# Kernel optimization log

Hardware: AMD Instinct MI355X
Metric: run time of the kernel (lower is better)

Reference implementation:

```python
import jax, jax.numpy as jnp
import numpy as np
import math

D_MODEL = 512
EXPAND = 2
D_INNER = EXPAND * D_MODEL          # 1024
HEADDIM = 8
NHEADS = D_INNER // HEADDIM         # 128
NGROUPS = 2
D_STATE = 16
CONV_DIM = D_INNER + 2 * NGROUPS * D_STATE   # 1088
D_IN_PROJ = 2 * D_INNER + 2 * NGROUPS * D_STATE + NHEADS  # 2240
P13 = [(0, 0), (1, 1)]
P31 = [(1, 1), (0, 0)]
P33 = [(1, 1), (1, 1)]


def silu(x):
    return x * jax.nn.sigmoid(x)


def dwconv(x, w, pad):
    # depthwise 2D conv; x: (B,C,H,W), w: (C,1,kh,kw)
    return jax.lax.conv_general_dilated(
        x, w, (1, 1), pad,
        dimension_numbers=('NCHW', 'OIHW', 'NCHW'),
        feature_group_count=x.shape[1])


def interleave_ch(a, b):
    # channel-interleave: out[:, ::2] = a, out[:, 1::2] = b
    Bn, C, Hh, Ww = a.shape
    return jnp.stack([a, b], axis=2).reshape(Bn, 2 * C, Hh, Ww)


def linear_attn(x, dt, A, Bm, Cm, Dp):
    # non-causal linear-attention duality of Mamba2 (grouped heads)
    # x: (B,L,h,p), dt: (B,L,h), A: (h,) negative, Bm/Cm: (B,L,g*ds), Dp: (h,)
    b, L, h, p = x.shape
    g, ds = NGROUPS, D_STATE
    dA = -(dt * A[None, None, :])          # ssd_positive_dA -> positive
    Vs = x * dA[..., None]
    K = Bm.reshape(b, L, g, ds)
    Q = Cm.reshape(b, L, g, ds)
    Vg = Vs.reshape(b, L, h // g, g, p)
    KV = jnp.einsum('blgs,blmgp->bmgsp', K, Vg)       # (b, h/g, g, ds, p)
    y = jnp.einsum('blgs,bmgsp->blmgp', Q, KV)        # (b, L, h/g, g, p)
    y = y + (x * Dp[None, None, :, None]).reshape(b, L, h // g, g, p)
    return y.reshape(b, L, h, p)


def setup_inputs() -> dict:
    key = jax.random.key(0)
    ks = jax.random.split(key, 20)
    Bn, Hh, Ww = 8, 64, 64
    L = Hh * Ww
    u = jax.random.normal(ks[0], (Bn, L, D_MODEL), jnp.float32)
    W_in = jax.random.normal(ks[1], (D_IN_PROJ, D_MODEL), jnp.float32) / math.sqrt(D_MODEL)
    dt = jnp.exp(jax.random.uniform(ks[2], (NHEADS,)) * (math.log(0.1) - math.log(0.001)) + math.log(0.001))
    dt = jnp.clip(dt, 1e-4, None)
    dt_bias = dt + jnp.log(-jnp.expm1(-dt))
    A_log = jnp.log(jax.random.uniform(ks[3], (NHEADS,), minval=1.0, maxval=16.0))
    Dp = jnp.ones((NHEADS,), jnp.float32)

    def cw(k, c, kh, kw):
        return jax.random.normal(k, (c, 1, kh, kw), jnp.float32) / math.sqrt(kh * kw)

    bcC = 2 * NGROUPS * D_STATE // 4  # 16
    w_conv2d = cw(ks[4], CONV_DIM // 2, 3, 3)
    w13x1 = cw(ks[5], D_INNER // 4, 1, 3)
    w31x1 = cw(ks[6], D_INNER // 4, 3, 1)
    w13x2 = cw(ks[7], D_INNER // 4, 1, 3)
    w31x2 = cw(ks[8], D_INNER // 4, 3, 1)
    w13bc1 = cw(ks[9], bcC, 1, 3)
    w31bc1 = cw(ks[10], bcC, 3, 1)
    w13bc2 = cw(ks[11], bcC, 1, 3)
    w31bc2 = cw(ks[12], bcC, 3, 1)
    w_conv2d_z = cw(ks[13], D_INNER, 3, 3)
    ln_g = jnp.ones((D_INNER,), jnp.float32)
    ln_b = jnp.zeros((D_INNER,), jnp.float32)
    scale = jnp.float32(1.0)
    shift = jnp.float32(0.0)
    alpha1 = jnp.float32(1.0)
    alpha2 = jnp.float32(1.0)
    W_out = jax.random.normal(ks[14], (D_MODEL, 2 * D_INNER), jnp.float32) / math.sqrt(2 * D_INNER)
    return dict(u=u, H=Hh, W=Ww, W_in=W_in, dt_bias=dt_bias, A_log=A_log, Dp=Dp,
                w_conv2d=w_conv2d, w13x1=w13x1, w31x1=w31x1, w13x2=w13x2, w31x2=w31x2,
                w13bc1=w13bc1, w31bc1=w31bc1, w13bc2=w13bc2, w31bc2=w31bc2,
                w_conv2d_z=w_conv2d_z, ln_g=ln_g, ln_b=ln_b, scale=scale, shift=shift,
                alpha1=alpha1, alpha2=alpha2, W_out=W_out)


def reference(u, H, W, W_in, dt_bias, A_log, Dp, w_conv2d, w13x1, w31x1, w13x2, w31x2,
              w13bc1, w31bc1, w13bc2, w31bc2, w_conv2d_z, ln_g, ln_b, scale, shift,
              alpha1, alpha2, W_out):
    Bn, L, _ = u.shape
    zxbcdt = u @ W_in.T                                 # (B,L,2240)
    z = zxbcdt[..., :D_INNER]
    xBC = zxbcdt[..., D_INNER:D_INNER + CONV_DIM]
    dt = zxbcdt[..., D_INNER + CONV_DIM:]
    dt = jax.nn.softplus(dt + dt_bias)                  # (B,L,h)

    # even/odd channel-interleave split, reshape to NCHW feature maps
    even = xBC[..., 0::2].reshape(Bn, H, W, -1).transpose(0, 3, 1, 2)
    odd = xBC[..., 1::2].reshape(Bn, H, W, -1).transpose(0, 3, 1, 2)
    even = silu(dwconv(even, w_conv2d, P33))

    oe = odd[:, 0::2]
    oo = odd[:, 1::2]
    x_oe, bc_oe = oe[:, :D_INNER // 4], oe[:, D_INNER // 4:]
    x_oo, bc_oo = oo[:, :D_INNER // 4], oo[:, D_INNER // 4:]
    x_oe = silu(dwconv(dwconv(x_oe, w31x1, P31), w13x1, P13))
    x_oo = silu(dwconv(dwconv(x_oo, w13x2, P13), w31x2, P31))
    bc_oe = silu(dwconv(dwconv(bc_oe, w13bc1, P13), w31bc1, P31))
    bc_oo = silu(dwconv(dwconv(bc_oo, w31bc2, P31), w13bc2, P13))
    xbc_oe = jnp.concatenate([x_oe, bc_oe], axis=1)
    xbc_oo = jnp.concatenate([x_oo, bc_oo], axis=1)
    odd = interleave_ch(xbc_oe, xbc_oo)

    xBCc = interleave_ch(even, odd)                     # (B, CONV_DIM, H, W)
    xBCc = xBCc.transpose(0, 2, 3, 1).reshape(Bn, L, CONV_DIM)
    x = xBCc[..., :D_INNER]
    Bm = xBCc[..., D_INNER:D_INNER + NGROUPS * D_STATE]
    Cm = xBCc[..., D_INNER + NGROUPS * D_STATE:]

    A = -jnp.exp(A_log)
    y = linear_attn(x.reshape(Bn, L, NHEADS, HEADDIM), dt, A, Bm, Cm, Dp)
    y = y.reshape(Bn, L, D_INNER)

    mu = y.mean(-1, keepdims=True)
    var = ((y - mu) ** 2).mean(-1, keepdims=True)
    y = (y - mu) / jnp.sqrt(var + 1e-5) * ln_g + ln_b
    y = y * scale + shift

    zc = z.reshape(Bn, H, W, D_INNER).transpose(0, 3, 1, 2)
    zc = silu(dwconv(zc, w_conv2d_z, P33))
    zc = zc.transpose(0, 2, 3, 1).reshape(Bn, L, D_INNER)

    out = jnp.concatenate([alpha1 * y, alpha2 * zc], axis=-1) @ W_out.T
    return out
```

## Files before the change

### kernel.cpp

```cpp
#include <hip/hip_runtime.h>
#include <hip/hip_bf16.h>
#include <cstdint>
#include <cstddef>

#define HDIM    64
#define WDIM    64
#define LPB     4096
#define DMODEL  512
#define DIN     1024
#define CONVD   1088
#define DPROJ   2240
#define NHEADS  128
#define NCV     2112

using f16    = _Float16;
using f16x4  = __attribute__((ext_vector_type(4))) _Float16;
using f16x8  = __attribute__((ext_vector_type(8))) _Float16;
using f32x4  = __attribute__((ext_vector_type(4))) float;

__device__ __forceinline__ float siluf(float x) { return x / (1.f + __expf(-x)); }
__device__ __forceinline__ float fsilu(float x) {
  return x * __builtin_amdgcn_rcpf(1.f + __expf(-x));
}

__device__ __forceinline__ void fma_mix_lo(float& acc, unsigned a, unsigned b) {
  asm("v_fma_mix_f32 %0, %1, %2, %0 op_sel_hi:[1,1,0]" : "+v"(acc) : "v"(a), "v"(b));
}
__device__ __forceinline__ void fma_mix_hi(float& acc, unsigned a, unsigned b) {
  asm("v_fma_mix_f32 %0, %1, %2, %0 op_sel:[1,1,0] op_sel_hi:[1,1,0]" : "+v"(acc) : "v"(a), "v"(b));
}
__device__ __forceinline__ void fmixl(float& acc, unsigned a, float b) {
  asm("v_fma_mix_f32 %0, %1, %2, %0 op_sel_hi:[1,0,0]" : "+v"(acc) : "v"(a), "v"(b));
}
__device__ __forceinline__ void fmixh(float& acc, unsigned a, float b) {
  asm("v_fma_mix_f32 %0, %1, %2, %0 op_sel:[1,0,0] op_sel_hi:[1,0,0]" : "+v"(acc) : "v"(a), "v"(b));
}

__global__ __launch_bounds__(256) void k_cvt(const float* __restrict__ in, f16* __restrict__ out) {
  size_t i = ((size_t)blockIdx.x * 256 + threadIdx.x) * 4;
  f32x4 v = *(const f32x4*)(in + i);
  f16x4 o;
  #pragma unroll
  for (int j = 0; j < 4; ++j) o[j] = (f16)v[j];
  *(f16x4*)(out + i) = o;
}

__global__ __launch_bounds__(256) void k_cvt_win(const float* __restrict__ W, f16* __restrict__ out) {
  int i = blockIdx.x * 256 + threadIdx.x;
  int row = i >> 9, col = i & 511;
  float v = (row < DPROJ) ? W[row * 512 + col] : 0.f;
  out[i] = (f16)v;
}

__global__ __launch_bounds__(256) void k_keff(const float* __restrict__ w33,
                       const float* __restrict__ w13x1, const float* __restrict__ w31x1,
                       const float* __restrict__ w13x2, const float* __restrict__ w31x2,
                       const float* __restrict__ w13bc1, const float* __restrict__ w31bc1,
                       const float* __restrict__ w13bc2, const float* __restrict__ w31bc2,
                       const float* __restrict__ wz,
                       f16* __restrict__ keffall) {
  int j = blockIdx.x * 256 + threadIdx.x;
  if (j >= NCV) return;
  if (j < 1024) {
    #pragma unroll
    for (int tap = 0; tap < 9; ++tap) keffall[tap * NCV + j] = (f16)wz[j * 9 + tap];
    return;
  }
  int jj = j - 1024;
  float kh[3] = {0,0,0}, kw[3] = {0,0,0};
  bool dense = ((jj & 1) == 0);
  if (!dense) {
    int m = jj >> 2;
    if ((jj & 3) == 1) {
      if (m < 256) { for (int t=0;t<3;++t){ kh[t]=w31x1[m*3+t];  kw[t]=w13x1[m*3+t];  } }
      else { int q=m-256; for (int t=0;t<3;++t){ kh[t]=w31bc1[q*3+t]; kw[t]=w13bc1[q*3+t]; } }
    } else {
      if (m < 256) { for (int t=0;t<3;++t){ kh[t]=w31x2[m*3+t];  kw[t]=w13x2[m*3+t];  } }
      else { int q=m-256; for (int t=0;t<3;++t){ kh[t]=w31bc2[q*3+t]; kw[t]=w13bc2[q*3+t]; } }
    }
  }
  #pragma unroll
  for (int dh = 0; dh < 3; ++dh)
    #pragma unroll
    for (int dw = 0; dw < 3; ++dw) {
      float v = dense ? w33[(jj >> 1) * 9 + dh*3 + dw] : kh[dh] * kw[dw];
      keffall[(dh*3 + dw) * NCV + j] = (f16)v;
    }
}

template<typename OutT>
__global__ __launch_bounds__(256) void k_gemmf(const f16* __restrict__ A, int lda,
                                               const f16* __restrict__ Bm, int ldb,
                                               OutT* __restrict__ C, int ldc,
                                               int Kseg, int NW, int ntn, int ntmn, long Cseg) {
  __shared__ __align__(16) f16 As[128 * 32];
  __shared__ __align__(16) f16 Bs[128 * 32];

  int nwg = gridDim.x, bid = blockIdx.x;
  int q = nwg >> 3, r = nwg & 7;
  int xcd = bid & 7, loc = bid >> 3;
  int wg  = (xcd < r ? xcd * (q + 1) : r * (q + 1) + (xcd - r) * q) + loc;
  int kseg = wg / ntmn;
  int rem  = wg - kseg * ntmn;
  long m0 = (long)(rem / ntn) * 128;
  long n0 = (long)(rem % ntn) * 128;
  const int kbase = kseg * Kseg;

  const int tid  = threadIdx.x;
  const int w    = tid >> 6, lane = tid & 63;
  const int wr   = w >> 1, wc = w & 1;

  f32x4 acc[4][4];
  #pragma unroll
  for (int i = 0; i < 4; ++i)
    #pragma unroll
    for (int j = 0; j < 4; ++j) acc[i][j] = (f32x4){0.f,0.f,0.f,0.f};

  const int srow = w * 16 + (lane >> 2);
  const int scol = (lane & 3) * 8;
  const long aoff = (m0 + srow) * (long)lda + scol + kbase;
  const long boff = (n0 + srow) * (long)ldb + scol + kbase;
  const int fr = lane & 15;
  const int kc = (lane >> 4) * 8;

  for (int k0 = 0; k0 < Kseg; k0 += 32) {
    #pragma unroll
    for (int i = 0; i < 2; ++i) {
      long ao = aoff + (long)i*64*lda + k0;
      long bo = boff + (long)i*64*ldb + k0;
      int ls = (i*4 + w) * 512;
      __builtin_amdgcn_global_load_lds((const __attribute__((address_space(1))) void*)(A + ao),
                                       (__attribute__((address_space(3))) void*)&As[ls], 16, 0, 0);
      __builtin_amdgcn_global_load_lds((const __attribute__((address_space(1))) void*)(Bm + bo),
                                       (__attribute__((address_space(3))) void*)&Bs[ls], 16, 0, 0);
    }
    __syncthreads();
    f16x8 af[4], bf[4];
    #pragma unroll
    for (int f = 0; f < 4; ++f) {
      af[f] = *(const f16x8*)&As[(wr*64 + f*16 + fr) * 32 + kc];
      bf[f] = *(const f16x8*)&Bs[(wc*64 + f*16 + fr) * 32 + kc];
    }
    #pragma unroll
    for (int i = 0; i < 4; ++i)
      #pragma unroll
      for (int j = 0; j < 4; ++j)
        acc[i][j] = __builtin_amdgcn_mfma_f32_16x16x32_f16(af[i], bf[j], acc[i][j], 0, 0, 0);
    __syncthreads();
  }

  OutT* Cb = C + (long)kseg * Cseg;
  const int cr = (lane >> 4) * 4;
  const int cc = lane & 15;
  #pragma unroll
  for (int i = 0; i < 4; ++i) {
    long rbase = m0 + wr*64 + i*16 + cr;
    #pragma unroll
    for (int j = 0; j < 4; ++j) {
      int col = (int)n0 + wc*64 + j*16 + cc;
      if (col < NW) {
        OutT* cp = Cb + rbase * (long)ldc + col;
        #pragma unroll
        for (int r = 0; r < 4; ++r) cp[(long)r * ldc] = (OutT)acc[i][j][r];
      }
    }
  }
}

__global__ __launch_bounds__(256) void k_red2h(const f16* __restrict__ part, long seg,
                                               float* __restrict__ out) {
  long i = ((long)blockIdx.x * 256 + threadIdx.x) * 4;
  f16x4 s0 = *(const f16x4*)(part + i);
  f16x4 s1 = *(const f16x4*)(part + seg + i);
  f32x4 o;
  #pragma unroll
  for (int j = 0; j < 4; ++j) o[j] = (float)s0[j] + (float)s1[j];
  *(f32x4*)(out + i) = o;
}

__global__ __launch_bounds__(192) void k_conv_all(const f16* __restrict__ zx,
                                                  const f16* __restrict__ keffall,
                                                  const float* __restrict__ a2_p,
                                                  const float* __restrict__ dt_bias,
                                                  const float* __restrict__ A_log,
                                                  f16* __restrict__ xbc,
                                                  f16* __restrict__ g2,
                                                  float* __restrict__ dAb) {
  int t = threadIdx.x;
  int bid = blockIdx.x, qq = gridDim.x >> 3;
  int l = (bid & 7) * qq + (bid >> 3);
  int h = (l >> 6) & 63, wq = l & 63;
  long rowbase = (long)l * DPROJ;

  if (t < 132) {
    int c0 = t * 8;
    int c1 = 1056 + t * 8;
    float acc0[8] = {0,0,0,0,0,0,0,0};
    float acc1[8] = {0,0,0,0,0,0,0,0};
    #pragma unroll
    for (int dh = 0; dh < 3; ++dh) {
      int hh = h + dh - 1;
      if (hh < 0 || hh >= HDIM) continue;
      #pragma unroll
      for (int dw = 0; dw < 3; ++dw) {
        int ww = wq + dw - 1;
        if (ww < 0 || ww >= WDIM) continue;
        long off = rowbase + (long)((dh-1)*WDIM + (dw-1)) * DPROJ;
        uint4 va = *(const uint4*)&zx[off + c0];
        uint4 vb = *(const uint4*)&zx[off + c1];
        uint4 wa = *(const uint4*)&keffall[(dh*3 + dw) * NCV + c0];
        uint4 wb = *(const uint4*)&keffall[(dh*3 + dw) * NCV + c1];
        fma_mix_lo(acc0[0], va.x, wa.x);  fma_mix_hi(acc0[1], va.x, wa.x);
        fma_mix_lo(acc1[0], vb.x, wb.x);  fma_mix_hi(acc1[1], vb.x, wb.x);
        fma_mix_lo(acc0[2], va.y, wa.y);  fma_mix_hi(acc0[3], va.y, wa.y);
        fma_mix_lo(acc1[2], vb.y, wb.y);  fma_mix_hi(acc1[3], vb.y, wb.y);
        fma_mix_lo(acc0[4], va.z, wa.z);  fma_mix_hi(acc0[5], va.z, wa.z);
        fma_mix_lo(acc1[4], vb.z, wb.z);  fma_mix_hi(acc1[5], vb.z, wb.z);
        fma_mix_lo(acc0[6], va.w, wa.w);  fma_mix_hi(acc0[7], va.w, wa.w);
        fma_mix_lo(acc1[6], vb.w, wb.w);  fma_mix_hi(acc1[7], vb.w, wb.w);
      }
    }
    float a2 = a2_p[0];
    {
      f16x8 o8;
      if (c0 < 1024) {
        #pragma unroll
        for (int j = 0; j < 8; ++j) o8[j] = (f16)(a2 * fsilu(acc0[j]));
        *(f16x8*)&g2[(long)l * 2048 + 1024 + c0] = o8;
      } else {
        #pragma unroll
        for (int j = 0; j < 8; ++j) o8[j] = (f16)fsilu(acc0[j]);
        *(f16x8*)&xbc[(long)l * CONVD + (c0 - 1024)] = o8;
      }
    }
    {
      f16x8 o8;
      #pragma unroll
      for (int j = 0; j < 8; ++j) o8[j] = (f16)fsilu(acc1[j]);
      *(f16x8*)&xbc[(long)l * CONVD + (c1 - 1024)] = o8;
    }
  } else if (t < 148) {
    int hd = (t - 132) * 8;
    f16x8 x = *(const f16x8*)&zx[rowbase + NCV + hd];
    f32x4 o0, o1;
    #pragma unroll
    for (int j = 0; j < 8; ++j) {
      float xx = (float)x[j] + dt_bias[hd + j];
      float sp = (xx > 20.f) ? xx : log1pf(__expf(xx));
      float dv = sp * __expf(A_log[hd + j]);
      if (j < 4) o0[j] = dv; else o1[j-4] = dv;
    }
    *(f32x4*)&dAb[(long)l * 128 + hd]     = o0;
    *(f32x4*)&dAb[(long)l * 128 + hd + 4] = o1;
  }
}

__global__ __launch_bounds__(512) void k_kv_part(const f16* __restrict__ xbc,
                                                 const float* __restrict__ dA,
                                                 float* __restrict__ part) {
  int t = threadIdx.x;
  int m = t >> 3, p = t & 7;
  int lc = blockIdx.x, b = blockIdx.y;
  float acc0[16], acc1[16];
  #pragma unroll
  for (int s = 0; s < 16; ++s) { acc0[s] = 0.f; acc1[s] = 0.f; }
  long lbase = (long)b * LPB + lc * 32;
  #pragma unroll 2
  for (int li = 0; li < 32; ++li) {
    long row = lbase + li;
    const f16* xr = xbc + row * CONVD;
    float2 aa = *(const float2*)&dA[row * 128 + 2*m];
    float xv0 = (float)xr[16*m + p]     * aa.x;
    float xv1 = (float)xr[16*m + 8 + p] * aa.y;
    uint4 q0 = *(const uint4*)(xr + DIN);
    uint4 q1 = *(const uint4*)(xr + DIN + 8);
    uint4 q2 = *(const uint4*)(xr + DIN + 16);
    uint4 q3 = *(const uint4*)(xr + DIN + 24);
    unsigned a0[4] = {q0.x, q0.y, q0.z, q0.w};
    unsigned a1[4] = {q1.x, q1.y, q1.z, q1.w};
    unsigned a2v[4] = {q2.x, q2.y, q2.z, q2.w};
    unsigned a3[4] = {q3.x, q3.y, q3.z, q3.w};
    #pragma unroll
    for (int k = 0; k < 4; ++k) {
      fmixl(acc0[2*k],     a0[k], xv0);  fmixh(acc0[2*k+1],     a0[k], xv0);
      fmixl(acc0[8+2*k],   a1[k], xv0);  fmixh(acc0[8+2*k+1],   a1[k], xv0);
      fmixl(acc1[2*k],     a2v[k], xv1); fmixh(acc1[2*k+1],     a2v[k], xv1);
      fmixl(acc1[8+2*k],   a3[k], xv1);  fmixh(acc1[8+2*k+1],   a3[k], xv1);
    }
  }
  long base = ((long)(b*128 + lc)) * 16384 + (long)m * 256;
  #pragma unroll
  for (int s = 0; s < 16; ++s) {
    part[base + s*8 + p]       = acc0[s];
    part[base + 128 + s*8 + p] = acc1[s];
  }
}

__global__ __launch_bounds__(256) void k_kv_red(const float* __restrict__ part,
                                                float* __restrict__ KV) {
  int e = blockIdx.x * 256 + threadIdx.x;
  int b = blockIdx.y;
  float s = 0.f;
  #pragma unroll 4
  for (int lc = 0; lc < 128; ++lc) s += part[((long)(b*128 + lc)) * 16384 + e];
  KV[(long)b * 16384 + e] = s;
}

__global__ __launch_bounds__(256) void k_y_ln(const f16* __restrict__ xbc,
                                              const float* __restrict__ KV,
                                              const float* __restrict__ Dp,
                                              const float* __restrict__ ln_g,
                                              const float* __restrict__ ln_b,
                                              const float* __restrict__ sc_p,
                                              const float* __restrict__ sh_p,
                                              const float* __restrict__ a1_p,
                                              f16* __restrict__ g2) {
  __shared__ float Qs[32][32];
  __shared__ float red[2][8];
  int t = threadIdx.x;
  int hd = t >> 1, pb = (t & 1) * 4;
  int m = hd >> 1, g = hd & 1;
  int b = blockIdx.x >> 7;
  long l0 = (long)b * LPB + (blockIdx.x & 127) * 32;

  f32x4 kv[16];
  #pragma unroll
  for (int s = 0; s < 16; ++s)
    kv[s] = *(const f32x4*)&KV[(long)b * 16384 + m*256 + g*128 + s*8 + pb];

  if (t < 128) {
    int tok = t >> 2, q8 = (t & 3) * 8;
    f16x8 qv = *(const f16x8*)&xbc[(l0 + tok) * CONVD + 1056 + q8];
    #pragma unroll
    for (int j = 0; j < 8; ++j) Qs[tok][q8 + j] = (float)qv[j];
  }
  int c0 = hd*8 + pb;
  f32x4 lg = *(const f32x4*)&ln_g[c0];
  f32x4 lb = *(const f32x4*)&ln_b[c0];
  float dpv = Dp[hd];
  float sc = sc_p[0], sh = sh_p[0], a1 = a1_p[0];
  int wv = t >> 6, lane = t & 63;
  __syncthreads();

  for (int tok = 0; tok < 32; ++tok) {
    long row = l0 + tok;
    f16x4 xr4 = *(const f16x4*)&xbc[row * CONVD + c0];
    f32x4 yv;
    #pragma unroll
    for (int j = 0; j < 4; ++j) yv[j] = (float)xr4[j] * dpv;
    #pragma unroll
    for (int s = 0; s < 16; ++s) {
      float qv = Qs[tok][g*16 + s];
      #pragma unroll
      for (int j = 0; j < 4; ++j) yv[j] = fmaf(qv, kv[s][j], yv[j]);
    }
    float s1 = yv[0] + yv[1] + yv[2] + yv[3];
    float s2 = yv[0]*yv[0] + yv[1]*yv[1] + yv[2]*yv[2] + yv[3]*yv[3];
    #pragma unroll
    for (int off = 1; off < 64; off <<= 1) {
      s1 += __shfl_xor(s1, off, 64);
      s2 += __shfl_xor(s2, off, 64);
    }
    if (lane == 0) { red[tok & 1][wv*2] = s1; red[tok & 1][wv*2 + 1] = s2; }
    __syncthreads();
    const float* rr = red[tok & 1];
    float S1 = rr[0] + rr[2] + rr[4] + rr[6];
    float S2 = rr[1] + rr[3] + rr[5] + rr[7];
    float mu   = S1 * (1.f/1024.f);
    float var  = S2 * (1.f/1024.f) - mu*mu;
    float rstd = rsqrtf(var + 1e-5f);
    f16x4 o4;
    #pragma unroll
    for (int j = 0; j < 4; ++j) {
      float yn = (yv[j] - mu) * rstd * lg[j] + lb[j];
      o4[j] = (f16)(a1 * (yn * sc + sh));
    }
    *(f16x4*)&g2[row * 2048 + c0] = o4;
  }
}

extern "C" void kernel_launch(void* const* d_in, const int* in_sizes, int n_in,
                              void* d_out, int out_size, void* d_ws, size_t ws_size,
                              hipStream_t stream) {
  const float* u       = (const float*)d_in[0];
  const float* W_in    = (const float*)d_in[3];
  const float* dt_bias = (const float*)d_in[4];
  const float* A_log   = (const float*)d_in[5];
  const float* Dp      = (const float*)d_in[6];
  const float* w33     = (const float*)d_in[7];
  const float* w13x1   = (const float*)d_in[8];
  const float* w31x1   = (const float*)d_in[9];
  const float* w13x2   = (const float*)d_in[10];
  const float* w31x2   = (const float*)d_in[11];
  const float* w13bc1  = (const float*)d_in[12];
  const float* w31bc1  = (const float*)d_in[13];
  const float* w13bc2  = (const float*)d_in[14];
  const float* w31bc2  = (const float*)d_in[15];
  const float* wz      = (const float*)d_in[16];
  const float* ln_g    = (const float*)d_in[17];
  const float* ln_b    = (const float*)d_in[18];
  const float* sc      = (const float*)d_in[19];
  const float* sh      = (const float*)d_in[20];
  const float* a1      = (const float*)d_in[21];
  const float* a2      = (const float*)d_in[22];
  const float* W_out   = (const float*)d_in[23];

  const size_t B_G2   = 16777216;
  const size_t B_ZX   = 18350080;
  const size_t B_XBC  = 8912896;
  const size_t B_DA   = 2097152;
  const size_t B_KV   = 65536;
  const size_t perC   = B_G2 + B_ZX + B_XBC + B_DA + B_KV;
  const size_t persist = 2359296 + 2097152 + 38912;

  int C = 8;
  while (C > 1 && persist + (size_t)C * perC > ws_size) C >>= 1;
  const int nch = 8 / C;
  const int Mc  = C * LPB;

  char* p = (char*)d_ws;
  f16*   win_f   = (f16*)p;   p += 2359296;
  f16*   wout_f  = (f16*)p;   p += 2097152;
  f16*   keffall = (f16*)p;   p += 38912;
  char*  arena   = p;
  f16*   g2      = (f16*)arena;
  f16*   u_f     = (f16*)arena;
  p = arena + (size_t)C * B_G2;
  f16*   zx      = (f16*)p;   p += (size_t)C * B_ZX;
  f16*   xbc     = (f16*)p;   p += (size_t)C * B_XBC;
  float* dAb     = (float*)p; p += (size_t)C * B_DA;
  float* KV      = (float*)p; p += (size_t)C * B_KV;
  float* part   = (float*)zx;
  f16*   kpart  = (f16*)zx;

  k_cvt_win<<<4608, 256, 0, stream>>>(W_in, win_f);
  k_cvt    <<<1024, 256, 0, stream>>>(W_out, wout_f);
  k_keff   <<<9, 256, 0, stream>>>(w33, w13x1, w31x1, w13x2, w31x2,
                                   w13bc1, w31bc1, w13bc2, w31bc2, wz, keffall);

  for (int ch = 0; ch < nch; ++ch) {
    const float* uc   = u + (size_t)ch * Mc * 512;
    float*       outc = (float*)d_out + (size_t)ch * Mc * 512;
    const int ntm = Mc / 128;

    k_cvt<<<Mc/2, 256, 0, stream>>>(uc, u_f);

    k_gemmf<f16><<<ntm*18, 256, 0, stream>>>(u_f, 512, win_f, 512,
                                             zx, DPROJ, 512, DPROJ, 18, ntm*18, 0);

    k_conv_all<<<Mc, 192, 0, stream>>>(zx, keffall, a2, dt_bias, A_log,
                                       xbc, g2, dAb);

    k_kv_part <<<dim3(128, C), 512, 0, stream>>>(xbc, dAb, part);
    k_kv_red  <<<dim3(64, C), 256, 0, stream>>>(part, KV);
    k_y_ln    <<<C*128, 256, 0, stream>>>(xbc, KV, Dp, ln_g, ln_b, sc, sh, a1, g2);

    const long cseg = (long)Mc * 512;
    k_gemmf<f16><<<ntm*4*2, 256, 0, stream>>>(g2, 2048, wout_f, 2048,
                                              kpart, 512, 1024, 512, 4, ntm*4, cseg);
    k_red2h<<<Mc/2, 256, 0, stream>>>(kpart, cseg, outc);
  }
}
```

Baseline: 573.8 us.

## Fuse input fp32-to-fp16 conversion into in-proj GEMM and compute two pixels per conv block

The in-projection GEMM now loads fp32 activations directly, converts them to fp16 in registers and writes them to shared memory. This removes the separate conversion kernel and its fp16 intermediate buffer, at the cost of losing the async global-to-LDS load path for the A operand. The depthwise conv kernel now handles two adjacent pixels per block, so overlapping input columns and conv weights are loaded once and reused, and the launch uses half as many blocks. The u_f alias on the g2 arena is dropped.

```diff
diff --git a/kernel.cpp b/kernel.cpp
--- a/kernel.cpp
+++ b/kernel.cpp
@@ -34,6 +34,13 @@
 }
 __device__ __forceinline__ void fmixh(float& acc, unsigned a, float b) {
   asm("v_fma_mix_f32 %0, %1, %2, %0 op_sel:[1,0,0] op_sel_hi:[1,0,0]" : "+v"(acc) : "v"(a), "v"(b));
+}
+
+__device__ __forceinline__ void fma8(float* acc, const uint4& v, const uint4& w) {
+  fma_mix_lo(acc[0], v.x, w.x);  fma_mix_hi(acc[1], v.x, w.x);
+  fma_mix_lo(acc[2], v.y, w.y);  fma_mix_hi(acc[3], v.y, w.y);
+  fma_mix_lo(acc[4], v.z, w.z);  fma_mix_hi(acc[5], v.z, w.z);
+  fma_mix_lo(acc[6], v.w, w.w);  fma_mix_hi(acc[7], v.w, w.w);
 }
 
 __global__ __launch_bounds__(256) void k_cvt(const float* __restrict__ in, f16* __restrict__ out) {
@@ -88,8 +95,8 @@
     }
 }
 
-template<typename OutT>
-__global__ __launch_bounds__(256) void k_gemmf(const f16* __restrict__ A, int lda,
+template<bool CVTA, typename OutT>
+__global__ __launch_bounds__(256) void k_gemmf(const void* __restrict__ Ap, int lda,
                                                const f16* __restrict__ Bm, int ldb,
                                                OutT* __restrict__ C, int ldc,
                                                int Kseg, int NW, int ntn, int ntmn, long Cseg) {
@@ -129,8 +136,18 @@
       long ao = aoff + (long)i*64*lda + k0;
       long bo = boff + (long)i*64*ldb + k0;
       int ls = (i*4 + w) * 512;
-      __builtin_amdgcn_global_load_lds((const __attribute__((address_space(1))) void*)(A + ao),
-                                       (__attribute__((address_space(3))) void*)&As[ls], 16, 0, 0);
+      if constexpr (CVTA) {
+        const float* ag = (const float*)Ap + ao;
+        f32x4 x0 = *(const f32x4*)ag;
+        f32x4 x1 = *(const f32x4*)(ag + 4);
+        f16x8 pk;
+        #pragma unroll
+        for (int j = 0; j < 4; ++j) { pk[j] = (f16)x0[j]; pk[4+j] = (f16)x1[j]; }
+        *(f16x8*)&As[ls + lane*8] = pk;
+      } else {
+        __builtin_amdgcn_global_load_lds((const __attribute__((address_space(1))) void*)((const f16*)Ap + ao),
+                                         (__attribute__((address_space(3))) void*)&As[ls], 16, 0, 0);
+      }
       __builtin_amdgcn_global_load_lds((const __attribute__((address_space(1))) void*)(Bm + bo),
                                        (__attribute__((address_space(3))) void*)&Bs[ls], 16, 0, 0);
     }
@@ -188,60 +205,75 @@
                                                   float* __restrict__ dAb) {
   int t = threadIdx.x;
   int bid = blockIdx.x, qq = gridDim.x >> 3;
-  int l = (bid & 7) * qq + (bid >> 3);
-  int h = (l >> 6) & 63, wq = l & 63;
-  long rowbase = (long)l * DPROJ;
+  int grp = (bid & 7) * qq + (bid >> 3);
+  int l0 = grp * 2;
+  long lb = (long)(l0 & ~(LPB - 1));
+  int h  = (l0 >> 6) & 63;
+  int w0 = l0 & 63;
 
   if (t < 132) {
     int c0 = t * 8;
-    int c1 = 1056 + t * 8;
-    float acc0[8] = {0,0,0,0,0,0,0,0};
-    float acc1[8] = {0,0,0,0,0,0,0,0};
+    int c1 = c0 + 1056;
+    float a00[8] = {0,0,0,0,0,0,0,0};
+    float a01[8] = {0,0,0,0,0,0,0,0};
+    float a10[8] = {0,0,0,0,0,0,0,0};
+    float a11[8] = {0,0,0,0,0,0,0,0};
+    const uint4 z4 = {0u,0u,0u,0u};
+
     #pragma unroll
     for (int dh = 0; dh < 3; ++dh) {
       int hh = h + dh - 1;
       if (hh < 0 || hh >= HDIM) continue;
+      const f16* rp = zx + (lb + (long)(hh * 64)) * DPROJ;
+      uint4 v0[4], v1[4];
+      #pragma unroll
+      for (int pp = 0; pp < 4; ++pp) {
+        int ww = w0 + pp - 1;
+        ww = ww < 0 ? 0 : (ww > 63 ? 63 : ww);
+        const f16* tp = rp + (long)ww * DPROJ;
+        v0[pp] = *(const uint4*)(tp + c0);
+        v1[pp] = *(const uint4*)(tp + c1);
+      }
+      if (w0 == 0)  { v0[0] = z4; v1[0] = z4; }
+      if (w0 == 62) { v0[3] = z4; v1[3] = z4; }
       #pragma unroll
       for (int dw = 0; dw < 3; ++dw) {
-        int ww = wq + dw - 1;
-        if (ww < 0 || ww >= WDIM) continue;
-        long off = rowbase + (long)((dh-1)*WDIM + (dw-1)) * DPROJ;
-        uint4 va = *(const uint4*)&zx[off + c0];
-        uint4 vb = *(const uint4*)&zx[off + c1];
         uint4 wa = *(const uint4*)&keffall[(dh*3 + dw) * NCV + c0];
         uint4 wb = *(const uint4*)&keffall[(dh*3 + dw) * NCV + c1];
-        fma_mix_lo(acc0[0], va.x, wa.x);  fma_mix_hi(acc0[1], va.x, wa.x);
-        fma_mix_lo(acc1[0], vb.x, wb.x);  fma_mix_hi(acc1[1], vb.x, wb.x);
-        fma_mix_lo(acc0[2], va.y, wa.y);  fma_mix_hi(acc0[3], va.y, wa.y);
-        fma_mix_lo(acc1[2], vb.y, wb.y);  fma_mix_hi(acc1[3], vb.y, wb.y);
-        fma_mix_lo(acc0[4], va.z, wa.z);  fma_mix_hi(acc0[5], va.z, wa.z);
-        fma_mix_lo(acc1[4], vb.z, wb.z);  fma_mix_hi(acc1[5], vb.z, wb.z);
-        fma_mix_lo(acc0[6], va.w, wa.w);  fma_mix_hi(acc0[7], va.w, wa.w);
-        fma_mix_lo(acc1[6], vb.w, wb.w);  fma_mix_hi(acc1[7], vb.w, wb.w);
+        fma8(a00, v0[dw],     wa);
+        fma8(a10, v0[dw + 1], wa);
+        fma8(a01, v1[dw],     wb);
+        fma8(a11, v1[dw + 1], wb);
       }
     }
+
     float a2 = a2_p[0];
-    {
+    #pragma unroll
+    for (int ti = 0; ti < 2; ++ti) {
+      long l = l0 + ti;
+      const float* pc0 = ti ? a10 : a00;
+      const float* pc1 = ti ? a11 : a01;
       f16x8 o8;
       if (c0 < 1024) {
         #pragma unroll
-        for (int j = 0; j < 8; ++j) o8[j] = (f16)(a2 * fsilu(acc0[j]));
-        *(f16x8*)&g2[(long)l * 2048 + 1024 + c0] = o8;
+        for (int j = 0; j < 8; ++j) o8[j] = (f16)(a2 * fsilu(pc0[j]));
+        *(f16x8*)&g2[l * 2048 + 1024 + c0] = o8;
       } else {
         #pragma unroll
-        for (int j = 0; j < 8; ++j) o8[j] = (f16)fsilu(acc0[j]);
-        *(f16x8*)&xbc[(long)l * CONVD + (c0 - 1024)] = o8;
+        for (int j = 0; j < 8; ++j) o8[j] = (f16)fsilu(pc0[j]);
+        *(f16x8*)&xbc[l * (long)CONVD + (c0 - 1024)] = o8;
       }
-    }
-    {
-      f16x8 o8;
+      f16x8 o9;
       #pragma unroll
-      for (int j = 0; j < 8; ++j) o8[j] = (f16)fsilu(acc1[j]);
-      *(f16x8*)&xbc[(long)l * CONVD + (c1 - 1024)] = o8;
-    }
-  } else if (t < 148) {
-    int hd = (t - 132) * 8;
-    f16x8 x = *(const f16x8*)&zx[rowbase + NCV + hd];
+      for (int j = 0; j < 8; ++j) o9[j] = (f16)fsilu(pc1[j]);
+      *(f16x8*)&xbc[l * (long)CONVD + (c1 - 1024)] = o9;
+    }
+  } else if (t < 164) {
+    int idx = t - 132;
+    int ti = idx >> 4;
+    int hd = (idx & 15) * 8;
+    long l = l0 + ti;
+    f16x8 x = *(const f16x8*)&zx[l * (long)DPROJ + NCV + hd];
     f32x4 o0, o1;
     #pragma unroll
     for (int j = 0; j < 8; ++j) {
@@ -250,8 +282,8 @@
       float dv = sp * __expf(A_log[hd + j]);
       if (j < 4) o0[j] = dv; else o1[j-4] = dv;
     }
-    *(f32x4*)&dAb[(long)l * 128 + hd]     = o0;
-    *(f32x4*)&dAb[(long)l * 128 + hd + 4] = o1;
+    *(f32x4*)&dAb[l * 128 + hd]     = o0;
+    *(f32x4*)&dAb[l * 128 + hd + 4] = o1;
   }
 }
 
@@ -422,10 +454,7 @@
   f16*   win_f   = (f16*)p;   p += 2359296;
   f16*   wout_f  = (f16*)p;   p += 2097152;
   f16*   keffall = (f16*)p;   p += 38912;
-  char*  arena   = p;
-  f16*   g2      = (f16*)arena;
-  f16*   u_f     = (f16*)arena;
-  p = arena + (size_t)C * B_G2;
+  f16*   g2      = (f16*)p;   p += (size_t)C * B_G2;
   f16*   zx      = (f16*)p;   p += (size_t)C * B_ZX;
   f16*   xbc     = (f16*)p;   p += (size_t)C * B_XBC;
   float* dAb     = (float*)p; p += (size_t)C * B_DA;
@@ -443,21 +472,19 @@
     float*       outc = (float*)d_out + (size_t)ch * Mc * 512;
     const int ntm = Mc / 128;
 
-    k_cvt<<<Mc/2, 256, 0, stream>>>(uc, u_f);
-
-    k_gemmf<f16><<<ntm*18, 256, 0, stream>>>(u_f, 512, win_f, 512,
-                                             zx, DPROJ, 512, DPROJ, 18, ntm*18, 0);
-
-    k_conv_all<<<Mc, 192, 0, stream>>>(zx, keffall, a2, dt_bias, A_log,
-                                       xbc, g2, dAb);
+    k_gemmf<true,f16><<<ntm*18, 256, 0, stream>>>((const void*)uc, 512, win_f, 512,
+                                                  zx, DPROJ, 512, DPROJ, 18, ntm*18, 0);
+
+    k_conv_all<<<Mc/2, 192, 0, stream>>>(zx, keffall, a2, dt_bias, A_log,
+                                         xbc, g2, dAb);
 
     k_kv_part <<<dim3(128, C), 512, 0, stream>>>(xbc, dAb, part);
     k_kv_red  <<<dim3(64, C), 256, 0, stream>>>(part, KV);
     k_y_ln    <<<C*128, 256, 0, stream>>>(xbc, KV, Dp, ln_g, ln_b, sc, sh, a1, g2);
 
     const long cseg = (long)Mc * 512;
-    k_gemmf<f16><<<ntm*4*2, 256, 0, stream>>>(g2, 2048, wout_f, 2048,
-                                              kpart, 512, 1024, 512, 4, ntm*4, cseg);
+    k_gemmf<false,f16><<<ntm*4*2, 256, 0, stream>>>((const void*)g2, 2048, wout_f, 2048,
+                                                    kpart, 512, 1024, 512, 4, ntm*4, cseg);
     k_red2h<<<Mc/2, 256, 0, stream>>>(kpart, cseg, outc);
   }
 }
```

After: 556.3 us. 1.03x faster.
